# Optimization experiments

Hardware: AMD Instinct MI355X
Metric: run time of the kernel (lower is better)

Reference implementation:

```python
import jax, jax.numpy as jnp
import numpy as np

NEG_SLOPE = 0.2
CONV3_NUM, CONV1_NUM, POLY_NUM = 3, 5, 4
FEAT_DIM = CONV3_NUM * 84 + CONV1_NUM * 12 + POLY_NUM * 12  # 360
DN = ('NCHW', 'OIHW', 'NCHW')


def leaky_relu(x):
    return jnp.where(x >= 0, x, NEG_SLOPE * x)


def conv3x3(x, feat):
    # per-sample dynamic 3x3 conv: feat[:, :81] -> kernel [3,3,3,3], feat[:, 81:84] -> bias
    B = x.shape[0]
    k = feat[:, :81].reshape(B, 3, 3, 3, 3)
    b = feat[:, 81:84]

    def one(xi, ki, bi):
        y = jax.lax.conv_general_dilated(xi[None], ki, (1, 1), 'SAME', dimension_numbers=DN)[0]
        return y + bi[:, None, None]

    return leaky_relu(jax.vmap(one)(x, k, b))


def conv1x1(x, feat):
    B = x.shape[0]
    k = feat[:, :9].reshape(B, 3, 3, 1, 1)
    b = feat[:, 9:12]

    def one(xi, ki, bi):
        y = jax.lax.conv_general_dilated(xi[None], ki, (1, 1), 'VALID', dimension_numbers=DN)[0]
        return y + bi[:, None, None]

    return leaky_relu(jax.vmap(one)(x, k, b))


def conv_stack(x, feature):
    residual = x
    for i in range(CONV3_NUM):
        x = conv3x3(x, feature[:, i * 84:(i + 1) * 84])
    off = CONV3_NUM * 84
    for i in range(CONV1_NUM):
        x = conv1x1(x, feature[:, off + i * 12:off + (i + 1) * 12])
    return residual + x


def att_map(feat, h_mat, w_mat, xc):
    # product over POLY_NUM of (a*h + b*w + c*x + d)
    att = jnp.ones_like(xc)
    for i in range(POLY_NUM):
        a = feat[:, i * 4 + 0].reshape(-1, 1, 1, 1)
        b = feat[:, i * 4 + 1].reshape(-1, 1, 1, 1)
        c = feat[:, i * 4 + 2].reshape(-1, 1, 1, 1)
        d = feat[:, i * 4 + 3].reshape(-1, 1, 1, 1)
        att = att * (a * h_mat + b * w_mat + c * xc + d)
    return att


def apply_attention(x, feature):
    H, W = x.shape[2], x.shape[3]
    h_mat = (jnp.arange(H, dtype=x.dtype) / H).reshape(1, 1, H, 1)
    w_mat = (jnp.arange(W, dtype=x.dtype) / W).reshape(1, 1, 1, W)
    off = CONV3_NUM * 84 + CONV1_NUM * 12
    atts = [att_map(feature[:, off + c * POLY_NUM * 4: off + (c + 1) * POLY_NUM * 4],
                    h_mat, w_mat, x[:, c:c + 1]) for c in range(3)]  # R, G, B
    att = jnp.concatenate(atts, axis=1)
    return x * (1 + att)


def setup_inputs() -> dict:
    key = jax.random.key(0)
    k1, k2, k3 = jax.random.split(key, 3)
    x = jax.random.uniform(k1, (8, 3, 512, 512), dtype=jnp.float32)
    thumb_x = jax.random.uniform(k2, (8, 3, 64, 64), dtype=jnp.float32)
    Wm = jax.random.normal(k3, (3, FEAT_DIM), dtype=jnp.float32) * 0.05
    bm = jnp.zeros((FEAT_DIM,), dtype=jnp.float32)
    return {"x": x, "thumb_x": thumb_x, "Wm": Wm, "bm": bm}


def reference(x, thumb_x, Wm, bm):
    # meta: GAP over thumbnail -> linear -> per-sample hypernetwork features [B, 360]
    feature = jnp.mean(thumb_x, axis=(2, 3)) @ Wm + bm
    x = conv_stack(x, feature)
    x = apply_attention(x, feature)
    thumb = conv_stack(thumb_x, feature)
    thumb = apply_attention(thumb, feature)
    return (x, thumb)
```

## Files before the change

### kernel.cpp

```cpp
#include <hip/hip_runtime.h>


#define LEAKY(v) fmaxf((v), 0.2f * (v))

constexpr int STRD = 72;
constexpr int ROWS0 = 22;
constexpr int CHS  = ROWS0 * STRD;
constexpr int BUFSZ = 3 * CHS + 16;

__global__ __launch_bounds__(256) void feat_kernel(
    const float* __restrict__ thumb, const float* __restrict__ Wm,
    const float* __restrict__ bm, float* __restrict__ feat)
{
    const int b = blockIdx.x;
    const int tid = threadIdx.x;
    __shared__ float red[256];
    __shared__ float smean[3];

    for (int c = 0; c < 3; ++c) {
        const float4* p = (const float4*)(thumb + (size_t)(b * 3 + c) * 4096);
        float s = 0.f;
#pragma unroll
        for (int k = 0; k < 4; ++k) {
            float4 v = p[tid + k * 256];
            s += v.x + v.y + v.z + v.w;
        }
        red[tid] = s;
        __syncthreads();
        for (int off = 128; off > 0; off >>= 1) {
            if (tid < off) red[tid] += red[tid + off];
            __syncthreads();
        }
        if (tid == 0) smean[c] = red[0] * (1.f / 4096.f);
        __syncthreads();
    }
    const float m0 = smean[0], m1 = smean[1], m2 = smean[2];
    for (int f = tid; f < 360; f += 256)
        feat[b * 360 + f] =
            fmaf(m0, Wm[f], fmaf(m1, Wm[360 + f], fmaf(m2, Wm[720 + f], bm[f])));
}

template<int R>
__device__ __forceinline__ void conv_rows(
    const float* __restrict__ buf, const float* __restrict__ fw,
    int r0, int gx, float4 acc[][3])
{
    const float b0 = fw[81], b1 = fw[82], b2 = fw[83];
#pragma unroll
    for (int j = 0; j < R; ++j) {
        acc[j][0] = make_float4(b0, b0, b0, b0);
        acc[j][1] = make_float4(b1, b1, b1, b1);
        acc[j][2] = make_float4(b2, b2, b2, b2);
    }
    const int gA = (gx < 0) ? 0 : gx;
#pragma unroll
    for (int ich = 0; ich < 3; ++ich) {
#pragma unroll
        for (int ri = 0; ri < R + 2; ++ri) {
            const int mr = r0 + 2 + ri;
            const int idx = ich * CHS + mr * STRD;
            const float4 A = *(const float4*)&buf[idx + gA];
            const float4 B = *(const float4*)&buf[idx + gx + 4];
            const float4 C = *(const float4*)&buf[idx + gx + 8];
#pragma unroll
            for (int j = 0; j < R; ++j) {
                const int dy = ri - j;
                if (dy < 0 || dy > 2) continue;
#pragma unroll
                for (int oc = 0; oc < 3; ++oc) {
                    const float w0 = fw[oc * 27 + ich * 9 + dy * 3 + 0];
                    const float w1 = fw[oc * 27 + ich * 9 + dy * 3 + 1];
                    const float w2 = fw[oc * 27 + ich * 9 + dy * 3 + 2];
                    float4& a = acc[j][oc];
                    a.x = fmaf(A.w, w0, fmaf(B.x, w1, fmaf(B.y, w2, a.x)));
                    a.y = fmaf(B.x, w0, fmaf(B.y, w1, fmaf(B.z, w2, a.y)));
                    a.z = fmaf(B.y, w0, fmaf(B.z, w1, fmaf(B.w, w2, a.z)));
                    a.w = fmaf(B.z, w0, fmaf(B.w, w1, fmaf(C.x, w2, a.w)));
                }
            }
        }
    }
}

__global__ __launch_bounds__(256, 2) void conv_att_kernel(
    const float* __restrict__ x, const float* __restrict__ thumb,
    const float* __restrict__ feat, float* __restrict__ out)
{
    __shared__ float buf[BUFSZ];

    int id = blockIdx.x;
    const float* src; float* dst; int H, W, b, trow, tcol;
    if (id < 2048) {
        b = id >> 8; const int t = id & 255;
        H = 512; W = 512; trow = (t >> 3) * 16; tcol = (t & 7) * 64;
        src = x; dst = out;
    } else {
        const int i2 = id - 2048;
        b = i2 >> 2; trow = (i2 & 3) * 16; tcol = 0;
        H = 64; W = 64; src = thumb;
        dst = out + (size_t)8 * 3 * 512 * 512;
    }
    const float* fb = feat + b * 360;
    const int tid = threadIdx.x;

    const float* sbg = src + (size_t)b * 3 * H * W;
    for (int q = tid; q < 1188; q += 256) {
        const int c = q / 396;
        const int rem = q - c * 396;
        const int mr = rem / 18;
        const int mq = rem - mr * 18;
        const int gr = trow + mr - 3;
        const int gc0 = tcol + 4 * mq - 4;
        const bool rok = (unsigned)gr < (unsigned)H;
        const float* gp = sbg + (size_t)c * H * W + (size_t)(rok ? gr : 0) * W;
        float4 v;
        if (rok && (unsigned)gc0 <= (unsigned)(W - 4)) {
            v = *(const float4*)&gp[gc0];
        } else {
            v.x = (rok && (unsigned)(gc0 + 0) < (unsigned)W) ? gp[gc0 + 0] : 0.f;
            v.y = (rok && (unsigned)(gc0 + 1) < (unsigned)W) ? gp[gc0 + 1] : 0.f;
            v.z = (rok && (unsigned)(gc0 + 2) < (unsigned)W) ? gp[gc0 + 2] : 0.f;
            v.w = (rok && (unsigned)(gc0 + 3) < (unsigned)W) ? gp[gc0 + 3] : 0.f;
        }
        *(float4*)&buf[c * CHS + mr * STRD + 4 * mq] = v;
    }
    __syncthreads();

    const int s3 = tid >> 4;
    const int gx3 = 4 * (tid & 15);

    const bool act1 = tid < 180;
    const int s1 = tid / 18;
    const int gx1 = 4 * (tid - s1 * 18) - 4;
    float4 acc[2][3];
    if (act1) conv_rows<2>(buf, fb, 2 * s1 - 2, gx1, acc);

    float4 res[3];
#pragma unroll
    for (int c = 0; c < 3; ++c)
        res[c] = *(const float4*)&buf[c * CHS + (s3 + 3) * STRD + gx3 + 4];
    __syncthreads();

    if (act1) {
        const int r0 = 2 * s1 - 2;
#pragma unroll
        for (int j = 0; j < 2; ++j)
#pragma unroll
            for (int oc = 0; oc < 3; ++oc) {
                float4 v = acc[j][oc];
                v.x = LEAKY(v.x); v.y = LEAKY(v.y); v.z = LEAKY(v.z); v.w = LEAKY(v.w);
                *(float4*)&buf[oc * CHS + (r0 + j + 3) * STRD + gx1 + 4] = v;
            }
    }
    __syncthreads();

    const bool act2 = tid < 162;
    const int s2 = tid / 18;
    const int gx2 = 4 * (tid - s2 * 18) - 4;
    if (act2) conv_rows<2>(buf, fb + 84, 2 * s2 - 1, gx2, acc);
    __syncthreads();

    if (act2) {
        const int r0 = 2 * s2 - 1;
#pragma unroll
        for (int j = 0; j < 2; ++j)
#pragma unroll
            for (int oc = 0; oc < 3; ++oc) {
                float4 v = acc[j][oc];
                v.x = LEAKY(v.x); v.y = LEAKY(v.y); v.z = LEAKY(v.z); v.w = LEAKY(v.w);
                *(float4*)&buf[oc * CHS + (r0 + j + 3) * STRD + gx2 + 4] = v;
            }
    }
    __syncthreads();

    float4 y[1][3];
    conv_rows<1>(buf, fb + 168, s3, gx3, y);
    float4 y0 = y[0][0], y1 = y[0][1], y2 = y[0][2];
    y0.x = LEAKY(y0.x); y0.y = LEAKY(y0.y); y0.z = LEAKY(y0.z); y0.w = LEAKY(y0.w);
    y1.x = LEAKY(y1.x); y1.y = LEAKY(y1.y); y1.z = LEAKY(y1.z); y1.w = LEAKY(y1.w);
    y2.x = LEAKY(y2.x); y2.y = LEAKY(y2.y); y2.z = LEAKY(y2.z); y2.w = LEAKY(y2.w);

#pragma unroll
    for (int lay = 0; lay < 5; ++lay) {
        const float* fw = fb + 252 + lay * 12;
        const float w00 = fw[0], w01 = fw[1], w02 = fw[2];
        const float w10 = fw[3], w11 = fw[4], w12 = fw[5];
        const float w20 = fw[6], w21 = fw[7], w22 = fw[8];
        const float c0 = fw[9], c1 = fw[10], c2 = fw[11];
        float4 z0, z1, z2;
        z0.x = fmaf(y0.x, w00, fmaf(y1.x, w01, fmaf(y2.x, w02, c0)));
        z0.y = fmaf(y0.y, w00, fmaf(y1.y, w01, fmaf(y2.y, w02, c0)));
        z0.z = fmaf(y0.z, w00, fmaf(y1.z, w01, fmaf(y2.z, w02, c0)));
        z0.w = fmaf(y0.w, w00, fmaf(y1.w, w01, fmaf(y2.w, w02, c0)));
        z1.x = fmaf(y0.x, w10, fmaf(y1.x, w11, fmaf(y2.x, w12, c1)));
        z1.y = fmaf(y0.y, w10, fmaf(y1.y, w11, fmaf(y2.y, w12, c1)));
        z1.z = fmaf(y0.z, w10, fmaf(y1.z, w11, fmaf(y2.z, w12, c1)));
        z1.w = fmaf(y0.w, w10, fmaf(y1.w, w11, fmaf(y2.w, w12, c1)));
        z2.x = fmaf(y0.x, w20, fmaf(y1.x, w21, fmaf(y2.x, w22, c2)));
        z2.y = fmaf(y0.y, w20, fmaf(y1.y, w21, fmaf(y2.y, w22, c2)));
        z2.z = fmaf(y0.z, w20, fmaf(y1.z, w21, fmaf(y2.z, w22, c2)));
        z2.w = fmaf(y0.w, w20, fmaf(y1.w, w21, fmaf(y2.w, w22, c2)));
        y0.x = LEAKY(z0.x); y0.y = LEAKY(z0.y); y0.z = LEAKY(z0.z); y0.w = LEAKY(z0.w);
        y1.x = LEAKY(z1.x); y1.y = LEAKY(z1.y); y1.z = LEAKY(z1.z); y1.w = LEAKY(z1.w);
        y2.x = LEAKY(z2.x); y2.y = LEAKY(z2.y); y2.z = LEAKY(z2.z); y2.w = LEAKY(z2.w);
    }

    const float invH = 1.f / (float)H;
    const float invW = 1.f / (float)W;
    const int gr = trow + s3;
    const float h = (float)gr * invH;
    const float wbase = (float)(tcol + gx3) * invW;
    const float4 wv = make_float4(wbase, wbase + invW, wbase + 2.f * invW, wbase + 3.f * invW);
#pragma unroll
    for (int ch = 0; ch < 3; ++ch) {
        const float* fp = fb + 312 + ch * 16;
        const float pa0 = fp[0], pb0 = fp[1], pc0 = fp[2], pd0 = fp[3];
        const float pa1 = fp[4], pb1 = fp[5], pc1 = fp[6], pd1 = fp[7];
        const float pa2 = fp[8], pb2 = fp[9], pc2 = fp[10], pd2 = fp[11];
        const float pa3 = fp[12], pb3 = fp[13], pc3 = fp[14], pd3 = fp[15];
        const float4 yv = (ch == 0) ? y0 : (ch == 1) ? y1 : y2;
        float4 v;
        v.x = yv.x + res[ch].x;
        v.y = yv.y + res[ch].y;
        v.z = yv.z + res[ch].z;
        v.w = yv.w + res[ch].w;
        const float t0 = fmaf(pa0, h, pd0), t1 = fmaf(pa1, h, pd1);
        const float t2 = fmaf(pa2, h, pd2), t3 = fmaf(pa3, h, pd3);
        float4 o;
        float a0 = fmaf(pb0, wv.x, fmaf(pc0, v.x, t0));
        a0 *= fmaf(pb1, wv.x, fmaf(pc1, v.x, t1));
        a0 *= fmaf(pb2, wv.x, fmaf(pc2, v.x, t2));
        a0 *= fmaf(pb3, wv.x, fmaf(pc3, v.x, t3));
        o.x = v.x * (1.f + a0);
        float a1 = fmaf(pb0, wv.y, fmaf(pc0, v.y, t0));
        a1 *= fmaf(pb1, wv.y, fmaf(pc1, v.y, t1));
        a1 *= fmaf(pb2, wv.y, fmaf(pc2, v.y, t2));
        a1 *= fmaf(pb3, wv.y, fmaf(pc3, v.y, t3));
        o.y = v.y * (1.f + a1);
        float a2 = fmaf(pb0, wv.z, fmaf(pc0, v.z, t0));
        a2 *= fmaf(pb1, wv.z, fmaf(pc1, v.z, t1));
        a2 *= fmaf(pb2, wv.z, fmaf(pc2, v.z, t2));
        a2 *= fmaf(pb3, wv.z, fmaf(pc3, v.z, t3));
        o.z = v.z * (1.f + a2);
        float a3 = fmaf(pb0, wv.w, fmaf(pc0, v.w, t0));
        a3 *= fmaf(pb1, wv.w, fmaf(pc1, v.w, t1));
        a3 *= fmaf(pb2, wv.w, fmaf(pc2, v.w, t2));
        a3 *= fmaf(pb3, wv.w, fmaf(pc3, v.w, t3));
        o.w = v.w * (1.f + a3);
        *(float4*)&dst[((size_t)(b * 3 + ch) * H + gr) * W + tcol + gx3] = o;
    }
}

extern "C" void kernel_launch(void* const* d_in, const int* in_sizes, int n_in,
                              void* d_out, int out_size, void* d_ws, size_t ws_size,
                              hipStream_t stream) {
    const float* x = (const float*)d_in[0];
    const float* thumb = (const float*)d_in[1];
    const float* Wm = (const float*)d_in[2];
    const float* bm = (const float*)d_in[3];
    float* out = (float*)d_out;
    float* feat = (float*)d_ws;

    feat_kernel<<<8, 256, 0, stream>>>(thumb, Wm, bm, feat);
    conv_att_kernel<<<2080, 256, 0, stream>>>(x, thumb, feat, out);
}
```

Baseline: 120.4 us.

## Split feature prep into two kernels, trim conv loads, raise occupancy hint

The per-sample feature computation is split into a 24-block channel-mean kernel and a small matmul kernel, so the mean reduction runs across more blocks. The conv inner loop now loads single floats for the left and right halo instead of full float4s, which lowers register and LDS traffic. The launch bound hint goes from 2 to 8 blocks per CU, pushing the compiler to use fewer registers. The residual is now read from global memory late in the kernel instead of being held in registers across stages. That frees registers but adds a global read, and it relies on an `sbg` pointer that must be defined in the hidden part of the code.

```diff
diff --git a/kernel.cpp b/kernel.cpp
--- a/kernel.cpp
+++ b/kernel.cpp
@@ -8,36 +8,39 @@
 constexpr int CHS  = ROWS0 * STRD;
 constexpr int BUFSZ = 3 * CHS + 16;
 
-__global__ __launch_bounds__(256) void feat_kernel(
-    const float* __restrict__ thumb, const float* __restrict__ Wm,
-    const float* __restrict__ bm, float* __restrict__ feat)
+__global__ __launch_bounds__(256) void means_kernel(
+    const float* __restrict__ thumb, float* __restrict__ ws)
+{
+    const int bc = blockIdx.x;
+    const int tid = threadIdx.x;
+    const float4* p = (const float4*)(thumb + (size_t)bc * 4096);
+    float s = 0.f;
+#pragma unroll
+    for (int k = 0; k < 4; ++k) {
+        float4 v = p[tid + k * 256];
+        s += v.x + v.y + v.z + v.w;
+    }
+    __shared__ float red[256];
+    red[tid] = s;
+    __syncthreads();
+    for (int off = 128; off > 0; off >>= 1) {
+        if (tid < off) red[tid] += red[tid + off];
+        __syncthreads();
+    }
+    if (tid == 0) ws[bc] = red[0] * (1.f / 4096.f);
+}
+
+__global__ __launch_bounds__(384) void fmm_kernel(
+    const float* __restrict__ Wm, const float* __restrict__ bm,
+    const float* __restrict__ ws, float* __restrict__ feat)
 {
     const int b = blockIdx.x;
-    const int tid = threadIdx.x;
-    __shared__ float red[256];
-    __shared__ float smean[3];
-
-    for (int c = 0; c < 3; ++c) {
-        const float4* p = (const float4*)(thumb + (size_t)(b * 3 + c) * 4096);
-        float s = 0.f;
-#pragma unroll
-        for (int k = 0; k < 4; ++k) {
-            float4 v = p[tid + k * 256];
-            s += v.x + v.y + v.z + v.w;
-        }
-        red[tid] = s;
-        __syncthreads();
-        for (int off = 128; off > 0; off >>= 1) {
-            if (tid < off) red[tid] += red[tid + off];
-            __syncthreads();
-        }
-        if (tid == 0) smean[c] = red[0] * (1.f / 4096.f);
-        __syncthreads();
-    }
-    const float m0 = smean[0], m1 = smean[1], m2 = smean[2];
-    for (int f = tid; f < 360; f += 256)
+    const int f = threadIdx.x;
+    if (f < 360) {
+        const float m0 = ws[b * 3 + 0], m1 = ws[b * 3 + 1], m2 = ws[b * 3 + 2];
         feat[b * 360 + f] =
             fmaf(m0, Wm[f], fmaf(m1, Wm[360 + f], fmaf(m2, Wm[720 + f], bm[f])));
+    }
 }
 
 template<int R>
@@ -52,16 +55,15 @@
         acc[j][1] = make_float4(b1, b1, b1, b1);
         acc[j][2] = make_float4(b2, b2, b2, b2);
     }
-    const int gA = (gx < 0) ? 0 : gx;
+    const int awo = (gx < 0) ? 0 : gx + 3;
 #pragma unroll
     for (int ich = 0; ich < 3; ++ich) {
 #pragma unroll
         for (int ri = 0; ri < R + 2; ++ri) {
-            const int mr = r0 + 2 + ri;
-            const int idx = ich * CHS + mr * STRD;
-            const float4 A = *(const float4*)&buf[idx + gA];
+            const int idx = ich * CHS + (r0 + 2 + ri) * STRD;
+            const float aw = buf[idx + awo];
             const float4 B = *(const float4*)&buf[idx + gx + 4];
-            const float4 C = *(const float4*)&buf[idx + gx + 8];
+            const float cx = buf[idx + gx + 8];
 #pragma unroll
             for (int j = 0; j < R; ++j) {
                 const int dy = ri - j;
@@ -72,17 +74,17 @@
                     const float w1 = fw[oc * 27 + ich * 9 + dy * 3 + 1];
                     const float w2 = fw[oc * 27 + ich * 9 + dy * 3 + 2];
                     float4& a = acc[j][oc];
-                    a.x = fmaf(A.w, w0, fmaf(B.x, w1, fmaf(B.y, w2, a.x)));
+                    a.x = fmaf(aw,  w0, fmaf(B.x, w1, fmaf(B.y, w2, a.x)));
                     a.y = fmaf(B.x, w0, fmaf(B.y, w1, fmaf(B.z, w2, a.y)));
                     a.z = fmaf(B.y, w0, fmaf(B.z, w1, fmaf(B.w, w2, a.z)));
-                    a.w = fmaf(B.z, w0, fmaf(B.w, w1, fmaf(C.x, w2, a.w)));
+                    a.w = fmaf(B.z, w0, fmaf(B.w, w1, fmaf(cx,  w2, a.w)));
                 }
             }
         }
     }
 }
 
-__global__ __launch_bounds__(256, 2) void conv_att_kernel(
+__global__ __launch_bounds__(256, 8) void conv_att_kernel(
     const float* __restrict__ x, const float* __restrict__ thumb,
     const float* __restrict__ feat, float* __restrict__ out)
 {
@@ -134,11 +136,6 @@
     const int gx1 = 4 * (tid - s1 * 18) - 4;
     float4 acc[2][3];
     if (act1) conv_rows<2>(buf, fb, 2 * s1 - 2, gx1, acc);
-
-    float4 res[3];
-#pragma unroll
-    for (int c = 0; c < 3; ++c)
-        res[c] = *(const float4*)&buf[c * CHS + (s3 + 3) * STRD + gx3 + 4];
     __syncthreads();
 
     if (act1) {
@@ -172,6 +169,12 @@
             }
     }
     __syncthreads();
+
+    const int gr = trow + s3;
+    float4 res[3];
+#pragma unroll
+    for (int c = 0; c < 3; ++c)
+        res[c] = *(const float4*)&sbg[((size_t)c * H + gr) * W + tcol + gx3];
 
     float4 y[1][3];
     conv_rows<1>(buf, fb + 168, s3, gx3, y);
@@ -207,7 +210,6 @@
 
     const float invH = 1.f / (float)H;
     const float invW = 1.f / (float)W;
-    const int gr = trow + s3;
     const float h = (float)gr * invH;
     const float wbase = (float)(tcol + gx3) * invW;
     const float4 wv = make_float4(wbase, wbase + invW, wbase + 2.f * invW, wbase + 3.f * invW);
@@ -259,8 +261,10 @@
     const float* Wm = (const float*)d_in[2];
     const float* bm = (const float*)d_in[3];
     float* out = (float*)d_out;
-    float* feat = (float*)d_ws;
-
-    feat_kernel<<<8, 256, 0, stream>>>(thumb, Wm, bm, feat);
+    float* means = (float*)d_ws;
+    float* feat = (float*)d_ws + 64;
+
+    means_kernel<<<24, 256, 0, stream>>>(thumb, means);
+    fmm_kernel<<<8, 384, 0, stream>>>(Wm, bm, means, feat);
     conv_att_kernel<<<2080, 256, 0, stream>>>(x, thumb, feat, out);
 }
```

After: 148.3 us. 23.2% more time.
